# Optimization experiments

Hardware: AMD Instinct MI355X
Metric: run time of the kernel (lower is better)

Reference implementation:

```python
import jax, jax.numpy as jnp
import numpy as np

N, C, H, W = 1, 1, 4096, 4096

def setup_inputs() -> dict:
    key = jax.random.key(0)
    x = jax.random.normal(key, (N, C, H, W), dtype=jnp.float32)
    return {"x": x}

def reference(x):
    # torch.median returns the lower of the two middle values for even counts:
    # take the k-th smallest with k = (n-1)//2.
    n = x.size
    median = jnp.sort(x.reshape(-1))[(n - 1) // 2]
    # threshold everything below the median to zero
    thresholded = jnp.where(x < median, jnp.float32(0.0), x)
    # 7x7 max pool, stride 1, padding 3 (torch pads with -inf for max pool)
    pooled = jax.lax.reduce_window(
        thresholded,
        -jnp.inf,
        jax.lax.max,
        window_dimensions=(1, 1, 7, 7),
        window_strides=(1, 1, 1, 1),
        padding=[(0, 0), (0, 0), (3, 3), (3, 3)],
    )
    # In the original, gather(flatten(thresholded), max_indices) == pooled,
    # so binarize where the thresholded value equals its local window max.
    binarized = jnp.where(thresholded == pooled, jnp.float32(1.0), jnp.float32(0.0))
    return binarized * x
```

## Files before the change

kernel.cpp:

```cpp
#include <hip/hip_runtime.h>
#include <math.h>

#define IMG_H 4096
#define IMG_W 4096
#define TS 64
#define HALO 3
#define TW 70
#define THS 71
#define HMS 65
#define NBINS 4096
#define CBLK 1024
#define CAPA 1024
#define CAND_MAX (1u<<22)
#define WLO (-0.001953125f)
#define WHI ( 0.001953125f)
#define RSLOT 32
#define MCAP 1024
#define NSUB 2048

struct SelState {
    unsigned bin;
    unsigned k_rem;
    float    median;
    unsigned flag;
};

__device__ __forceinline__ unsigned f2u(float f) {
    unsigned b = __float_as_uint(f);
    unsigned mask = (unsigned)(-(int)(b >> 31)) | 0x80000000u;
    return b ^ mask;
}
__device__ __forceinline__ float u2f(unsigned u) {
    unsigned mask = (u >> 31) ? 0x80000000u : 0xFFFFFFFFu;
    return __uint_as_float(u ^ mask);
}

__device__ __forceinline__ int val_bin(float v) {
    float t = (v + 4.0f) * 512.0f;
    int b = (int)t;
    b = b < 0 ? 0 : b;
    b = b > (NBINS - 1) ? (NBINS - 1) : b;
    return b;
}

__device__ __forceinline__ int sub_bin(float v) {
    float t = (v - WLO) * (float)(NSUB * 256);
    int b = (int)t;
    b = b < 0 ? 0 : b;
    b = b > (NSUB - 1) ? (NSUB - 1) : b;
    return b;
}

__global__ __launch_bounds__(512) void count_compact(
    const float4* __restrict__ x4, int n4,
    unsigned* __restrict__ belowArr,
    unsigned* __restrict__ candA, unsigned* __restrict__ cntA)
{
    __shared__ unsigned buf[CAPA];
    __shared__ unsigned wred[8];
    __shared__ unsigned lcnt, gbase;
    const int t = threadIdx.x;
    if (t == 0) lcnt = 0;
    __syncthreads();

    unsigned below = 0;
    int idx = blockIdx.x * 512 + t;
    int stride = gridDim.x * 512;
    for (int i = idx; i < n4; i += stride) {
        float4 v = x4[i];
        float vs[4] = {v.x, v.y, v.z, v.w};
        #pragma unroll
        for (int j = 0; j < 4; j++) {
            float vv = vs[j];
            below += (vv < WLO) ? 1u : 0u;
            if (vv >= WLO && vv < WHI) {
                unsigned p = atomicAdd(&lcnt, 1u);
                unsigned key = f2u(vv);
                if (p < CAPA) buf[p] = key;
                else { unsigned q = atomicAdd(cntA, 1u); if (q < CAND_MAX) candA[q] = key; }
            }
        }
    }
    #pragma unroll
    for (int off = 32; off >= 1; off >>= 1) below += __shfl_down(below, off, 64);
    if ((t & 63) == 0) wred[t >> 6] = below;
    __syncthreads();
    if (t == 0) {
        unsigned tot = 0;
        #pragma unroll
        for (int w = 0; w < 8; w++) tot += wred[w];
        belowArr[blockIdx.x] = tot;
        gbase = atomicAdd(cntA, (lcnt > CAPA) ? CAPA : lcnt);
    }
    __syncthreads();
    unsigned m = lcnt; if (m > CAPA) m = CAPA;
    for (unsigned i = t; i < m; i += 512) {
        unsigned q = gbase + i;
        if (q < CAND_MAX) candA[q] = buf[i];
    }
}

__global__ __launch_bounds__(1024) void finalize_kernel(
    const unsigned* __restrict__ belowArr,
    const unsigned* __restrict__ candA, const unsigned* __restrict__ cntA,
    unsigned K, SelState* __restrict__ st)
{
    __shared__ unsigned hist[NSUB];
    __shared__ unsigned mem[MCAP];
    __shared__ unsigned wsum[16];
    __shared__ unsigned s_below, s_sb, s_kr2, mcnt;
    const int t = threadIdx.x;
    const unsigned lane = t & 63, wid = t >> 6;

    unsigned b = (t < CBLK) ? belowArr[t] : 0u;
    #pragma unroll
    for (int off = 32; off >= 1; off >>= 1) b += __shfl_down(b, off, 64);
    if (lane == 0) wsum[wid] = b;
    if (t == 0) mcnt = 0;
    __syncthreads();
    if (t == 0) {
        unsigned tot = 0;
        #pragma unroll
        for (int w = 0; w < 16; w++) tot += wsum[w];
        s_below = tot;
    }
    __syncthreads();

    const unsigned below = s_below;
    const unsigned M = *cntA;
    const bool direct = (K >= below) && (K - below < M) && (M <= RSLOT * 1024u);
    if (!direct) return;

    const unsigned kRem = K - below;

    unsigned rc[RSLOT];
    #pragma unroll
    for (int j = 0; j < RSLOT; j++) {
        int i = j * 1024 + t;
        rc[j] = (i < (int)M) ? candA[i] : 0u;
    }
    for (int i = t; i < NSUB; i += 1024) hist[i] = 0;
    __syncthreads();

    #pragma unroll
    for (int j = 0; j < RSLOT; j++) {
        int i = j * 1024 + t;
        if (i < (int)M) atomicAdd(&hist[sub_bin(u2f(rc[j]))], 1u);
    }
    __syncthreads();

    unsigned d0 = hist[t * 2], d1 = hist[t * 2 + 1];
    unsigned loc2 = d0 + d1;
    unsigned s2 = loc2;
    #pragma unroll
    for (int off = 1; off < 64; off <<= 1) {
        unsigned u = __shfl_up(s2, off, 64);
        if (lane >= off) s2 += u;
    }
    if (lane == 63) wsum[wid] = s2;
    __syncthreads();
    unsigned base2 = 0;
    for (unsigned w = 0; w < wid; w++) base2 += wsum[w];
    unsigned excl2 = base2 + s2 - loc2;
    if (kRem >= excl2 && kRem < excl2 + loc2) {
        if (kRem < excl2 + d0) { s_sb = (unsigned)(t * 2);     s_kr2 = kRem - excl2; }
        else                   { s_sb = (unsigned)(t * 2 + 1); s_kr2 = kRem - excl2 - d0; }
    }
    __syncthreads();

    const int sb = (int)s_sb;
    #pragma unroll
    for (int j = 0; j < RSLOT; j++) {
        int i = j * 1024 + t;
        if (i < (int)M && sub_bin(u2f(rc[j])) == sb) {
            unsigned p = atomicAdd(&mcnt, 1u);
            if (p < MCAP) mem[p] = rc[j];
        }
    }
    __syncthreads();
    if (mcnt > MCAP) return;

    const unsigned m = mcnt;
    const unsigned kr2 = s_kr2;
    if ((unsigned)t < m) {
        unsigned ku = mem[t];
        unsigned c = 0, e = 0;
        for (unsigned j = 0; j < m; j++) {
            unsigned kj = mem[j];
            c += (kj < ku);
            e += (kj == ku);
        }
        if (c <= kr2 && kr2 < c + e) { st->median = u2f(ku); st->flag = 1; }
    }
}

__global__ __launch_bounds__(1024) void fb_exact(
    const float4* __restrict__ x4, int n4, unsigned K,
    unsigned* __restrict__ candB, SelState* __restrict__ st)
{
    if (st->flag) return;
    __shared__ unsigned lh[NBINS];
    __shared__ unsigned wsum[16];
    __shared__ unsigned s_bin, s_krem, s_m, s_pref, s_kr;
    const int t = threadIdx.x;
    const unsigned lane = t & 63, wid = t >> 6;

    for (int i = t; i < NBINS; i += 1024) lh[i] = 0;
    __syncthreads();
    for (int i = t; i < n4; i += 1024) {
        float4 v = x4[i];
        atomicAdd(&lh[val_bin(v.x)], 1u);
        atomicAdd(&lh[val_bin(v.y)], 1u);
        atomicAdd(&lh[val_bin(v.z)], 1u);
        atomicAdd(&lh[val_bin(v.w)], 1u);
    }
    __syncthreads();

    {
        unsigned cb[4];
        unsigned local = 0;
        #pragma unroll
        for (int j = 0; j < 4; j++) { cb[j] = lh[t * 4 + j]; local += cb[j]; }
        unsigned s = local;
        #pragma unroll
        for (int off = 1; off < 64; off <<= 1) {
            unsigned u = __shfl_up(s, off, 64);
            if (lane >= off) s += u;
        }
        if (lane == 63) wsum[wid] = s;
        __syncthreads();
        unsigned base = 0;
        for (unsigned w = 0; w < wid; w++) base += wsum[w];
        unsigned excl = base + s - local;
        if (K >= excl && K < excl + local) {
            unsigned cum = excl;
            #pragma unroll
            for (int j = 0; j < 4; j++) {
                if (K < cum + cb[j]) { s_bin = (unsigned)(t * 4 + j); s_krem = K - cum; break; }
                cum += cb[j];
            }
        }
        if (t == 0) s_m = 0;
        __syncthreads();
    }

    {
        const int b = (int)s_bin;
        for (int i = t; i < n4; i += 1024) {
            float4 v = x4[i];
            float vs[4] = {v.x, v.y, v.z, v.w};
            #pragma unroll
            for (int j = 0; j < 4; j++) {
                if (val_bin(vs[j]) == b) {
                    unsigned p = atomicAdd(&s_m, 1u);
                    candB[p] = f2u(vs[j]);
                }
            }
        }
        __syncthreads();
    }

    const int M = (int)s_m;
    if (t == 0) { s_pref = 0; s_kr = s_krem; }
    for (int p = 0; p < 3; p++) {
        const int shift = (p == 0) ? 21 : ((p == 1) ? 10 : 0);
        const int bits  = (p == 2) ? 10 : 11;
        const int nb    = 1 << bits;
        for (int i = t; i < nb; i += 1024) lh[i] = 0;
        __syncthreads();
        const unsigned pref = s_pref;
        for (int i = t; i < M; i += 1024) {
            unsigned u = candB[i];
            bool ok = (p == 0) || ((u >> ((p == 1) ? 21 : 10)) == pref);
            if (ok) atomicAdd(&lh[(u >> shift) & (unsigned)(nb - 1)], 1u);
        }
        __syncthreads();
        const int P = nb >> 10;
        unsigned c0 = lh[t * (P ? P : 1)];
        unsigned c1 = (P == 2) ? lh[t * 2 + 1] : 0u;
        unsigned valid = (P >= 1) || (t < nb);
        if (P == 0) { c0 = (t < nb) ? lh[t] : 0u; c1 = 0u; }
        unsigned local = valid ? (c0 + c1) : 0u;
        unsigned s = local;
        #pragma unroll
        for (int off = 1; off < 64; off <<= 1) {
            unsigned u = __shfl_up(s, off, 64);
            if (lane >= off) s += u;
        }
        if (lane == 63) wsum[wid] = s;
        __syncthreads();
        unsigned base = 0;
        for (unsigned w = 0; w < wid; w++) base += wsum[w];
        unsigned excl = base + s - local;
        unsigned kRem = s_kr;
        __syncthreads();
        if (kRem >= excl && kRem < excl + local) {
            if (P == 2) {
                if (kRem < excl + c0) { s_pref = (pref << bits) | (unsigned)(t * 2);     s_kr = kRem - excl; }
                else                  { s_pref = (pref << bits) | (unsigned)(t * 2 + 1); s_kr = kRem - excl - c0; }
            } else {
                s_pref = (pref << bits) | (unsigned)t;
                s_kr = kRem - excl;
            }
        }
        __syncthreads();
    }
    if (t == 0) st->median = u2f(s_pref);
}

__global__ __launch_bounds__(512) void nms_kernel(
    const float* __restrict__ x, float* __restrict__ out,
    const SelState* __restrict__ st)
{
    __shared__ float th[TW * THS];
    __shared__ float hm[TW * HMS];

    const float med = st->median;
    const float NEGINF = -__builtin_inff();
    const int bx = blockIdx.x, by = blockIdx.y;
    const int gy0 = by * TS - HALO;
    const int gcol0 = bx * TS - 4;

    for (int task = threadIdx.x; task < TW * 18; task += 512) {
        int r = task / 18, q = task - r * 18;
        int gy = gy0 + r;
        int gxb = gcol0 + q * 4;
        bool rowok = (gy >= 0 && gy < IMG_H);
        float vs[4];
        if (rowok && gxb >= 0 && gxb + 4 <= IMG_W) {
            float4 v = *(const float4*)&x[gy * IMG_W + gxb];
            vs[0] = v.x; vs[1] = v.y; vs[2] = v.z; vs[3] = v.w;
        } else if (rowok) {
            #pragma unroll
            for (int cmp = 0; cmp < 4; cmp++) {
                int gx = gxb + cmp;
                vs[cmp] = (gx >= 0 && gx < IMG_W) ? x[gy * IMG_W + gx] : NEGINF;
            }
        } else {
            vs[0] = vs[1] = vs[2] = vs[3] = NEGINF;
        }
        #pragma unroll
        for (int cmp = 0; cmp < 4; cmp++) {
            int c = q * 4 - 1 + cmp;
            if ((unsigned)c < (unsigned)TW) {
                float v = vs[cmp];
                v = (v == NEGINF) ? v : ((v < med) ? 0.0f : v);
                th[r * THS + c] = v;
            }
        }
    }
    __syncthreads();

    for (int task = threadIdx.x; task < TW * 8; task += 512) {
        int r = task % TW;
        int c0 = (task / TW) * 8;
        float w[7];
        #pragma unroll
        for (int i = 0; i < 14; i++) {
            w[i % 7] = th[r * THS + c0 + i];
            if (i >= 6) {
                float m = w[0];
                #pragma unroll
                for (int k = 1; k < 7; k++) m = fmaxf(m, w[k]);
                hm[r * HMS + c0 + i - 6] = m;
            }
        }
    }
    __syncthreads();

    {
        const int c = threadIdx.x & 63;
        const int rr0 = (threadIdx.x >> 6) * 8;
        float w[7];
        #pragma unroll
        for (int i = 0; i < 14; i++) {
            w[i % 7] = hm[(rr0 + i) * HMS + c];
            if (i >= 6) {
                int R = rr0 + i - 6;
                float m = w[0];
                #pragma unroll
                for (int k = 1; k < 7; k++) m = fmaxf(m, w[k]);
                float t = th[(R + HALO) * THS + (c + HALO)];
                int gy = by * TS + R;
                int gx = bx * TS + c;
                float o = 0.0f;
                if (t == m) {
                    o = (t != 0.0f) ? t : x[gy * IMG_W + gx];
                }
                out[gy * IMG_W + gx] = o;
            }
        }
    }
}

extern "C" void kernel_launch(void* const* d_in, const int* in_sizes, int n_in,
                              void* d_out, int out_size, void* d_ws, size_t ws_size,
                              hipStream_t stream)
{
    const float* x = (const float*)d_in[0];
    float* out = (float*)d_out;
    const int n = in_sizes[0];
    const unsigned K = (unsigned)((n - 1) / 2);

    char* ws = (char*)d_ws;
    unsigned* cntA     = (unsigned*)ws;
    SelState* st       = (SelState*)(ws + 16);
    unsigned* belowArr = (unsigned*)(ws + 256);
    unsigned* candA    = (unsigned*)(ws + ws_size / 2);

    hipMemsetAsync(d_ws, 0, 32, stream);

    const int n4 = n / 4;
    count_compact<<<CBLK, 512, 0, stream>>>((const float4*)x, n4, belowArr, candA, cntA);
    finalize_kernel<<<1, 1024, 0, stream>>>(belowArr, candA, cntA, K, st);
    fb_exact<<<1, 1024, 0, stream>>>((const float4*)x, n4, K, (unsigned*)d_out, st);

    dim3 fg(IMG_W / TS, IMG_H / TS);
    nms_kernel<<<fg, 512, 0, stream>>>(x, out, st);
}
```

Baseline: 149.2 us.

## Vectorize NMS tile loads, row/column max passes and stores with float4

Rewrites the max-pool/NMS kernel to use float4 accesses throughout. The shared tile keeps an extra left column so it is 16-byte aligned, and the row strides are padded to multiples of 4. The horizontal pass reads 16 floats as four vector loads. The vertical pass now has each thread produce 2 rows by 4 columns, sharing the middle 6-row max, and write float4 outputs. Separately, finalize now always writes the flag so the memset shrinks to the counter only, and the kernel sets launch bounds for occupancy; the padded strides may bring back LDS bank conflicts.

```diff
diff --git a/kernel.cpp b/kernel.cpp
--- a/kernel.cpp
+++ b/kernel.cpp
@@ -6,8 +6,8 @@
 #define TS 64
 #define HALO 3
 #define TW 70
-#define THS 71
-#define HMS 65
+#define THS 76
+#define HMS 68
 #define NBINS 4096
 #define CBLK 1024
 #define CAPA 1024
@@ -108,7 +108,8 @@
     __shared__ unsigned hist[NSUB];
     __shared__ unsigned mem[MCAP];
     __shared__ unsigned wsum[16];
-    __shared__ unsigned s_below, s_sb, s_kr2, mcnt;
+    __shared__ unsigned s_below, s_sb, s_kr2, mcnt, s_found;
+    __shared__ float s_med;
     const int t = threadIdx.x;
     const unsigned lane = t & 63, wid = t >> 6;
 
@@ -116,7 +117,7 @@
     #pragma unroll
     for (int off = 32; off >= 1; off >>= 1) b += __shfl_down(b, off, 64);
     if (lane == 0) wsum[wid] = b;
-    if (t == 0) mcnt = 0;
+    if (t == 0) { mcnt = 0; s_found = 0; }
     __syncthreads();
     if (t == 0) {
         unsigned tot = 0;
@@ -129,7 +130,10 @@
     const unsigned below = s_below;
     const unsigned M = *cntA;
     const bool direct = (K >= below) && (K - below < M) && (M <= RSLOT * 1024u);
-    if (!direct) return;
+    if (!direct) {
+        if (t == 0) st->flag = 0;
+        return;
+    }
 
     const unsigned kRem = K - below;
 
@@ -178,19 +182,25 @@
         }
     }
     __syncthreads();
-    if (mcnt > MCAP) return;
-
-    const unsigned m = mcnt;
-    const unsigned kr2 = s_kr2;
-    if ((unsigned)t < m) {
-        unsigned ku = mem[t];
-        unsigned c = 0, e = 0;
-        for (unsigned j = 0; j < m; j++) {
-            unsigned kj = mem[j];
-            c += (kj < ku);
-            e += (kj == ku);
-        }
-        if (c <= kr2 && kr2 < c + e) { st->median = u2f(ku); st->flag = 1; }
+
+    if (mcnt <= MCAP) {
+        const unsigned m = mcnt;
+        const unsigned kr2 = s_kr2;
+        if ((unsigned)t < m) {
+            unsigned ku = mem[t];
+            unsigned c = 0, e = 0;
+            for (unsigned j = 0; j < m; j++) {
+                unsigned kj = mem[j];
+                c += (kj < ku);
+                e += (kj == ku);
+            }
+            if (c <= kr2 && kr2 < c + e) { s_med = u2f(ku); s_found = 1; }
+        }
+    }
+    __syncthreads();
+    if (t == 0) {
+        if (s_found) st->median = s_med;
+        st->flag = s_found;
     }
 }
 
@@ -276,11 +286,9 @@
         }
         __syncthreads();
         const int P = nb >> 10;
-        unsigned c0 = lh[t * (P ? P : 1)];
+        unsigned c0 = (P == 2) ? lh[t * 2] : lh[t];
         unsigned c1 = (P == 2) ? lh[t * 2 + 1] : 0u;
-        unsigned valid = (P >= 1) || (t < nb);
-        if (P == 0) { c0 = (t < nb) ? lh[t] : 0u; c1 = 0u; }
-        unsigned local = valid ? (c0 + c1) : 0u;
+        unsigned local = c0 + c1;
         unsigned s = local;
         #pragma unroll
         for (int off = 1; off < 64; off <<= 1) {
@@ -308,7 +316,7 @@
     if (t == 0) st->median = u2f(s_pref);
 }
 
-__global__ __launch_bounds__(512) void nms_kernel(
+__global__ __launch_bounds__(512, 8) void nms_kernel(
     const float* __restrict__ x, float* __restrict__ out,
     const SelState* __restrict__ st)
 {
@@ -319,76 +327,84 @@
     const float NEGINF = -__builtin_inff();
     const int bx = blockIdx.x, by = blockIdx.y;
     const int gy0 = by * TS - HALO;
-    const int gcol0 = bx * TS - 4;
+    const int gxbase = bx * TS - 4;
 
     for (int task = threadIdx.x; task < TW * 18; task += 512) {
         int r = task / 18, q = task - r * 18;
         int gy = gy0 + r;
-        int gxb = gcol0 + q * 4;
-        bool rowok = (gy >= 0 && gy < IMG_H);
-        float vs[4];
-        if (rowok && gxb >= 0 && gxb + 4 <= IMG_W) {
-            float4 v = *(const float4*)&x[gy * IMG_W + gxb];
-            vs[0] = v.x; vs[1] = v.y; vs[2] = v.z; vs[3] = v.w;
-        } else if (rowok) {
-            #pragma unroll
-            for (int cmp = 0; cmp < 4; cmp++) {
-                int gx = gxb + cmp;
-                vs[cmp] = (gx >= 0 && gx < IMG_W) ? x[gy * IMG_W + gx] : NEGINF;
-            }
+        int gxb = gxbase + q * 4;
+        float4 v;
+        if (gy >= 0 && gy < IMG_H && gxb >= 0 && gxb < IMG_W) {
+            v = *(const float4*)&x[gy * IMG_W + gxb];
+            v.x = (v.x < med) ? 0.0f : v.x;
+            v.y = (v.y < med) ? 0.0f : v.y;
+            v.z = (v.z < med) ? 0.0f : v.z;
+            v.w = (v.w < med) ? 0.0f : v.w;
         } else {
-            vs[0] = vs[1] = vs[2] = vs[3] = NEGINF;
-        }
-        #pragma unroll
-        for (int cmp = 0; cmp < 4; cmp++) {
-            int c = q * 4 - 1 + cmp;
-            if ((unsigned)c < (unsigned)TW) {
-                float v = vs[cmp];
-                v = (v == NEGINF) ? v : ((v < med) ? 0.0f : v);
-                th[r * THS + c] = v;
-            }
-        }
+            v = make_float4(NEGINF, NEGINF, NEGINF, NEGINF);
+        }
+        *(float4*)&th[r * THS + q * 4] = v;
     }
     __syncthreads();
 
     for (int task = threadIdx.x; task < TW * 8; task += 512) {
         int r = task % TW;
         int c0 = (task / TW) * 8;
-        float w[7];
-        #pragma unroll
-        for (int i = 0; i < 14; i++) {
-            w[i % 7] = th[r * THS + c0 + i];
-            if (i >= 6) {
-                float m = w[0];
-                #pragma unroll
-                for (int k = 1; k < 7; k++) m = fmaxf(m, w[k]);
-                hm[r * HMS + c0 + i - 6] = m;
-            }
-        }
+        float f[16];
+        *(float4*)&f[0]  = *(const float4*)&th[r * THS + c0];
+        *(float4*)&f[4]  = *(const float4*)&th[r * THS + c0 + 4];
+        *(float4*)&f[8]  = *(const float4*)&th[r * THS + c0 + 8];
+        *(float4*)&f[12] = *(const float4*)&th[r * THS + c0 + 12];
+        float o[8];
+        #pragma unroll
+        for (int i = 0; i < 8; i++) {
+            float m = f[i + 1];
+            #pragma unroll
+            for (int k = 2; k <= 7; k++) m = fmaxf(m, f[i + k]);
+            o[i] = m;
+        }
+        *(float4*)&hm[r * HMS + c0]     = make_float4(o[0], o[1], o[2], o[3]);
+        *(float4*)&hm[r * HMS + c0 + 4] = make_float4(o[4], o[5], o[6], o[7]);
     }
     __syncthreads();
 
     {
-        const int c = threadIdx.x & 63;
-        const int rr0 = (threadIdx.x >> 6) * 8;
-        float w[7];
-        #pragma unroll
-        for (int i = 0; i < 14; i++) {
-            w[i % 7] = hm[(rr0 + i) * HMS + c];
-            if (i >= 6) {
-                int R = rr0 + i - 6;
-                float m = w[0];
-                #pragma unroll
-                for (int k = 1; k < 7; k++) m = fmaxf(m, w[k]);
-                float t = th[(R + HALO) * THS + (c + HALO)];
-                int gy = by * TS + R;
-                int gx = bx * TS + c;
+        const int cg  = threadIdx.x & 15;
+        const int rr0 = (threadIdx.x >> 4) * 2;
+        const int cb  = cg * 4;
+
+        float4 h0  = *(const float4*)&hm[(rr0 + 0) * HMS + cb];
+        float4 mid = *(const float4*)&hm[(rr0 + 1) * HMS + cb];
+        #pragma unroll
+        for (int i = 2; i <= 6; i++) {
+            float4 hi = *(const float4*)&hm[(rr0 + i) * HMS + cb];
+            mid.x = fmaxf(mid.x, hi.x); mid.y = fmaxf(mid.y, hi.y);
+            mid.z = fmaxf(mid.z, hi.z); mid.w = fmaxf(mid.w, hi.w);
+        }
+        float4 h7 = *(const float4*)&hm[(rr0 + 7) * HMS + cb];
+
+        #pragma unroll
+        for (int k = 0; k < 2; k++) {
+            int R = rr0 + k;
+            float4 e = (k == 0) ? h0 : h7;
+            float m4[4];
+            m4[0] = fmaxf(mid.x, e.x); m4[1] = fmaxf(mid.y, e.y);
+            m4[2] = fmaxf(mid.z, e.z); m4[3] = fmaxf(mid.w, e.w);
+            float4 t4 = *(const float4*)&th[(R + HALO) * THS + cb + 4];
+            float tt[4] = {t4.x, t4.y, t4.z, t4.w};
+            int gy = by * TS + R;
+            int gx = bx * TS + cb;
+            float o4[4];
+            #pragma unroll
+            for (int c = 0; c < 4; c++) {
                 float o = 0.0f;
-                if (t == m) {
-                    o = (t != 0.0f) ? t : x[gy * IMG_W + gx];
+                if (tt[c] == m4[c]) {
+                    o = (tt[c] != 0.0f) ? tt[c] : x[gy * IMG_W + gx + c];
                 }
-                out[gy * IMG_W + gx] = o;
-            }
+                o4[c] = o;
+            }
+            *(float4*)&out[gy * IMG_W + gx] =
+                make_float4(o4[0], o4[1], o4[2], o4[3]);
         }
     }
 }
@@ -408,7 +424,7 @@
     unsigned* belowArr = (unsigned*)(ws + 256);
     unsigned* candA    = (unsigned*)(ws + ws_size / 2);
 
-    hipMemsetAsync(d_ws, 0, 32, stream);
+    hipMemsetAsync(cntA, 0, 4, stream);
 
     const int n4 = n / 4;
     count_compact<<<CBLK, 512, 0, stream>>>((const float4*)x, n4, belowArr, candA, cntA);
```

New measurement: 149.2 us. No clear change (+0.0%).
